# Kernel optimization log

Hardware: AMD Instinct MI355X
Metric: run time of the kernel (lower is better)

The kernel has to match this reference:

```python
import jax, jax.numpy as jnp
import numpy as np

B, T, S, H = 4, 256, 1024, 256


def setup_inputs() -> dict:
    key = jax.random.key(0)
    k1, k2, k3, k4, k5, k6 = jax.random.split(key, 6)
    query = jax.random.normal(k1, (B, T, H), dtype=jnp.float32)
    encoder_outputs = jax.random.normal(k2, (B, S, H), dtype=jnp.float32)
    src_lengths = jax.random.randint(k3, (B,), 1, S + 1).astype(jnp.int64)
    scale = 1.0 / np.sqrt(H)
    W_h = jax.random.normal(k4, (H, H), dtype=jnp.float32) * scale
    W_s = jax.random.normal(k5, (H, H), dtype=jnp.float32) * scale
    v = jax.random.normal(k6, (H,), dtype=jnp.float32) * scale
    return {
        "query": query,
        "encoder_outputs": encoder_outputs,
        "src_lengths": src_lengths,
        "W_h": W_h,
        "W_s": W_s,
        "v": v,
    }


def reference(query, encoder_outputs, src_lengths, W_h, W_s, v):
    # score(h_i, s_j) = v^T tanh(W_h h_i + W_s s_j)
    # project once per sequence, then broadcast-add over (tgt, src)
    q_proj = jnp.einsum("bth,hk->btk", query, W_h)            # (B, T, H)
    e_proj = jnp.einsum("bsh,hk->bsk", encoder_outputs, W_s)  # (B, S, H)
    # (B, T, S, H) additive intermediate -> reduce with v
    feats = jnp.tanh(q_proj[:, :, None, :] + e_proj[:, None, :, :])
    scores = jnp.einsum("btsh,h->bts", feats, v)              # (B, T, S)
    # mask padding positions (src positions >= src_lengths[b])
    valid = jnp.arange(scores.shape[-1])[None, :] < src_lengths[:, None]  # (B, S)
    scores = jnp.where(valid[:, None, :], scores, jnp.finfo(scores.dtype).min)
    attn = jax.nn.softmax(scores, axis=-1)                    # (B, T, S)
    attn_out = jnp.einsum("bts,bsh->bth", attn, encoder_outputs)  # (B, T, H)
    return attn_out
```

## Files before the change

### kernel.cpp

```cpp
#include <hip/hip_runtime.h>
#include <math.h>

#define NB 4
#define NT 256
#define NS 1024
#define NH 256
#define TT 2
#define SBK 128
#define NSQ (NS / SBK)
#define BS (NB * NS)

static constexpr float CTWO   = 2.8853900817779268f;
static constexpr float LOG2E  = 1.4426950408889634f;
static constexpr float ACLAMP = 62.0f;

__global__ __launch_bounds__(256) void proj_kernel(const float* __restrict__ Q,
                                                   const float* __restrict__ E,
                                                   const float* __restrict__ W_h,
                                                   const float* __restrict__ W_s,
                                                   float* __restrict__ tq,
                                                   float* __restrict__ te4) {
  __shared__ float As[32][68];
  __shared__ float Bs[32][68];
  const int tid = threadIdx.x;
  int r0 = blockIdx.x * 64;
  const int n0 = blockIdx.y * 64;
  const bool is_q = (r0 < NB * NT);
  const float* A;
  const float* W;
  if (is_q) { A = Q; W = W_h; }
  else      { A = E; W = W_s; r0 -= NB * NT; }
  const int tx = tid & 15;
  const int ty = tid >> 4;
  float acc[4][4] = {};
  for (int k0 = 0; k0 < NH; k0 += 32) {
    {
      const int r = tid >> 2;
      const int kq = (tid & 3) * 8;
      const float* src = A + (size_t)(r0 + r) * NH + k0 + kq;
      float4 v0 = *(const float4*)(src);
      float4 v1 = *(const float4*)(src + 4);
      As[kq + 0][r] = v0.x; As[kq + 1][r] = v0.y; As[kq + 2][r] = v0.z; As[kq + 3][r] = v0.w;
      As[kq + 4][r] = v1.x; As[kq + 5][r] = v1.y; As[kq + 6][r] = v1.z; As[kq + 7][r] = v1.w;
    }
    {
      const int k = tid >> 3;
      const int nq = (tid & 7) * 8;
      const float* src = W + (size_t)(k0 + k) * NH + n0 + nq;
      *(float4*)&Bs[k][nq]     = *(const float4*)(src);
      *(float4*)&Bs[k][nq + 4] = *(const float4*)(src + 4);
    }
    __syncthreads();
    #pragma unroll
    for (int k = 0; k < 32; ++k) {
      float4 a = *(const float4*)&As[k][ty * 4];
      float4 b = *(const float4*)&Bs[k][tx * 4];
      const float av[4] = {a.x, a.y, a.z, a.w};
      const float bv[4] = {b.x, b.y, b.z, b.w};
      #pragma unroll
      for (int i = 0; i < 4; ++i)
        #pragma unroll
        for (int j = 0; j < 4; ++j)
          acc[i][j] = fmaf(av[i], bv[j], acc[i][j]);
    }
    __syncthreads();
  }
  #pragma unroll
  for (int i = 0; i < 4; ++i) {
    float vals[4];
    #pragma unroll
    for (int j = 0; j < 4; ++j) {
      float x = acc[i][j] * CTWO;
      x = fminf(fmaxf(x, -ACLAMP), ACLAMP);
      vals[j] = __builtin_amdgcn_exp2f(x);
    }
    const int r = r0 + ty * 4 + i;
    if (is_q) {
      #pragma unroll
      for (int j = 0; j < 4; ++j)
        tq[(size_t)r * NH + n0 + tx * 4 + j] = vals[j];
    } else {
      const int h4 = (n0 >> 2) + tx;
      float4 w = {vals[0], vals[1], vals[2], vals[3]};
      *(float4*)&te4[((size_t)h4 * BS + r) * 4] = w;
    }
  }
}

#define PAIR(qa, ea, va, qb, eb, vb, ACC)                                  \
  {                                                                        \
    float ta = fmaf((qa), (ea), 1.0f);                                     \
    float tb = fmaf((qb), (eb), 1.0f);                                     \
    float num = fmaf((va), tb, (vb) * ta);                                 \
    float den = ta * tb;                                                   \
    ACC = fmaf(num, __builtin_amdgcn_rcpf(den), ACC);                      \
  }

__global__ __launch_bounds__(256) void attn_main_kernel(
    const float4* __restrict__ tqq,
    const float4* __restrict__ te4q,
    const float4* __restrict__ enc4,
    const int* __restrict__ src_len,
    const float4* __restrict__ vq,
    float4* __restrict__ po4, float* __restrict__ mbuf, float* __restrict__ lbuf) {
  __shared__ float p_lds[4][TT][SBK];
  const int tid = threadIdx.x;
  const int wid = tid >> 6;
  const int lane = tid & 63;
  const int bx = blockIdx.x;
  const int sq = wid * 2 + (bx & 1);
  const int b  = (bx >> 1) & 3;
  const int tt = bx >> 3;
  const int btbase = b * NT + tt * TT;
  const int s0 = sq * SBK;
  const int len = src_len[b];

  if (s0 >= len) {
    if (lane < TT) {
      mbuf[(size_t)(btbase + lane) * NSQ + sq] = -INFINITY;
      lbuf[(size_t)(btbase + lane) * NSQ + sq] = 0.f;
    }
    return;
  }

  float sumv;
  {
    float4 v4 = vq[lane];
    float sv = (v4.x + v4.y) + (v4.z + v4.w);
    #pragma unroll
    for (int o = 32; o > 0; o >>= 1) sv += __shfl_xor(sv, o, 64);
    sumv = sv;
  }

  const int gs0 = b * NS + s0;
  const int sa = s0 + lane;
  const int sb = s0 + 64 + lane;
  const bool va_ok = sa < len;
  const bool vb_ok = sb < len;

  float accA0[TT], accA1[TT], accB0[TT], accB1[TT];
  #pragma unroll
  for (int t = 0; t < TT; ++t) { accA0[t] = accA1[t] = accB0[t] = accB1[t] = 0.f; }

  #pragma unroll 4
  for (int h4 = 0; h4 < NH / 4; ++h4) {
    const float4 ea = te4q[(size_t)h4 * BS + gs0 + lane];
    const float4 eb = te4q[(size_t)h4 * BS + gs0 + 64 + lane];
    const float4 vv = vq[h4];
    #pragma unroll
    for (int t = 0; t < TT; ++t) {
      const float4 q = tqq[(size_t)(btbase + t) * (NH / 4) + h4];
      PAIR(q.x, ea.x, vv.x, q.y, ea.y, vv.y, accA0[t]);
      PAIR(q.z, ea.z, vv.z, q.w, ea.w, vv.w, accA1[t]);
      PAIR(q.x, eb.x, vv.x, q.y, eb.y, vv.y, accB0[t]);
      PAIR(q.z, eb.z, vv.z, q.w, eb.w, vv.w, accB1[t]);
    }
  }

  #pragma unroll
  for (int t = 0; t < TT; ++t) {
    float xa = va_ok ? fmaf(-2.f, accA0[t] + accA1[t], sumv) : -INFINITY;
    float xb = vb_ok ? fmaf(-2.f, accB0[t] + accB1[t], sumv) : -INFINITY;
    float m = fmaxf(xa, xb);
    #pragma unroll
    for (int o = 32; o > 0; o >>= 1) m = fmaxf(m, __shfl_xor(m, o, 64));
    float pa = __builtin_amdgcn_exp2f((xa - m) * LOG2E);
    float pb = __builtin_amdgcn_exp2f((xb - m) * LOG2E);
    float l = pa + pb;
    #pragma unroll
    for (int o = 32; o > 0; o >>= 1) l += __shfl_xor(l, o, 64);
    p_lds[wid][t][lane] = pa;
    p_lds[wid][t][64 + lane] = pb;
    if (lane == 0) {
      mbuf[(size_t)(btbase + t) * NSQ + sq] = m;
      lbuf[(size_t)(btbase + t) * NSQ + sq] = l;
    }
  }

  float4 o[TT];
  #pragma unroll
  for (int t = 0; t < TT; ++t) o[t] = make_float4(0.f, 0.f, 0.f, 0.f);
  #pragma unroll 2
  for (int s = 0; s < SBK; s += 4) {
    float4 e0 = enc4[(size_t)(gs0 + s + 0) * (NH / 4) + lane];
    float4 e1 = enc4[(size_t)(gs0 + s + 1) * (NH / 4) + lane];
    float4 e2 = enc4[(size_t)(gs0 + s + 2) * (NH / 4) + lane];
    float4 e3 = enc4[(size_t)(gs0 + s + 3) * (NH / 4) + lane];
    #pragma unroll
    for (int t = 0; t < TT; ++t) {
      float4 p = *(const float4*)&p_lds[wid][t][s];
      o[t].x = fmaf(p.x, e0.x, o[t].x); o[t].y = fmaf(p.x, e0.y, o[t].y);
      o[t].z = fmaf(p.x, e0.z, o[t].z); o[t].w = fmaf(p.x, e0.w, o[t].w);
      o[t].x = fmaf(p.y, e1.x, o[t].x); o[t].y = fmaf(p.y, e1.y, o[t].y);
      o[t].z = fmaf(p.y, e1.z, o[t].z); o[t].w = fmaf(p.y, e1.w, o[t].w);
      o[t].x = fmaf(p.z, e2.x, o[t].x); o[t].y = fmaf(p.z, e2.y, o[t].y);
      o[t].z = fmaf(p.z, e2.z, o[t].z); o[t].w = fmaf(p.z, e2.w, o[t].w);
      o[t].x = fmaf(p.w, e3.x, o[t].x); o[t].y = fmaf(p.w, e3.y, o[t].y);
      o[t].z = fmaf(p.w, e3.z, o[t].z); o[t].w = fmaf(p.w, e3.w, o[t].w);
    }
  }
  #pragma unroll
  for (int t = 0; t < TT; ++t)
    po4[((size_t)(btbase + t) * NSQ + sq) * (NH / 4) + lane] = o[t];
}

__global__ __launch_bounds__(256) void combine_kernel(const float* __restrict__ po,
                                                      const float* __restrict__ mbuf,
                                                      const float* __restrict__ lbuf,
                                                      float* __restrict__ out) {
  const int bt = blockIdx.x;
  const int h = threadIdx.x;
  float m[NSQ], l[NSQ];
  float M = -INFINITY;
  #pragma unroll
  for (int i = 0; i < NSQ; ++i) {
    m[i] = mbuf[(size_t)bt * NSQ + i];
    l[i] = lbuf[(size_t)bt * NSQ + i];
    M = fmaxf(M, m[i]);
  }
  float L = 0.f, o = 0.f;
  #pragma unroll
  for (int i = 0; i < NSQ; ++i) {
    if (m[i] > -INFINITY) {
      float w = __builtin_amdgcn_exp2f((m[i] - M) * LOG2E);
      L = fmaf(w, l[i], L);
      o = fmaf(w, po[((size_t)bt * NSQ + i) * NH + h], o);
    }
  }
  out[(size_t)bt * NH + h] = o / L;
}

extern "C" void kernel_launch(void* const* d_in, const int* in_sizes, int n_in,
                              void* d_out, int out_size, void* d_ws, size_t ws_size,
                              hipStream_t stream) {
  const float* query = (const float*)d_in[0];
  const float* enc   = (const float*)d_in[1];
  const int*   slen  = (const int*)d_in[2];
  const float* W_h   = (const float*)d_in[3];
  const float* W_s   = (const float*)d_in[4];
  const float* v     = (const float*)d_in[5];
  float* out = (float*)d_out;

  float* ws = (float*)d_ws;
  float* tq  = ws;
  float* te4 = tq + (size_t)NB * NT * NH;
  float* po  = te4 + (size_t)NB * NS * NH;
  float* mb  = po + (size_t)NB * NT * NSQ * NH;
  float* lb  = mb + (size_t)NB * NT * NSQ;

  hipLaunchKernelGGL(proj_kernel, dim3((NB * (NT + NS)) / 64, NH / 64), dim3(256), 0, stream,
                     query, enc, W_h, W_s, tq, te4);
  hipLaunchKernelGGL(attn_main_kernel, dim3(NB * (NT / TT) * NSQ / 4), dim3(256), 0, stream,
                     (const float4*)tq, (const float4*)te4, (const float4*)enc, slen,
                     (const float4*)v, (float4*)po, mb, lb);
  hipLaunchKernelGGL(combine_kernel, dim3(NB * NT), dim3(256), 0, stream, po, mb, lb, out);
}
```

Baseline: 73.88 us.

## Share encoder tiles across waves via LDS with direct global-to-LDS loads

Each block now covers 8 target rows and one source chunk, with its four waves sharing the same encoder projection and encoder tiles. Those tiles are staged in a 32 KB LDS buffer through global_load_lds, so each one is fetched once per block rather than once per wave. Block indexing is remapped so batches and source chunks interleave across the grid, and launch bounds now request 4 blocks per CU. The cost is extra barriers, higher LDS use that can lower occupancy, and a single buffer with no overlap between loads and compute.

Result: slower. 209.7 us (+183.9%).

```diff
diff --git a/kernel.cpp b/kernel.cpp
--- a/kernel.cpp
+++ b/kernel.cpp
@@ -5,6 +5,7 @@
 #define NT 256
 #define NS 1024
 #define NH 256
+#define BT 8
 #define TT 2
 #define SBK 128
 #define NSQ (NS / SBK)
@@ -13,6 +14,9 @@
 static constexpr float CTWO   = 2.8853900817779268f;
 static constexpr float LOG2E  = 1.4426950408889634f;
 static constexpr float ACLAMP = 62.0f;
+
+typedef __attribute__((address_space(1))) const void GAS;
+typedef __attribute__((address_space(3))) void LAS;
 
 __global__ __launch_bounds__(256) void proj_kernel(const float* __restrict__ Q,
                                                    const float* __restrict__ E,
@@ -96,29 +100,34 @@
     ACC = fmaf(num, __builtin_amdgcn_rcpf(den), ACC);                      \
   }
 
-__global__ __launch_bounds__(256) void attn_main_kernel(
+__global__ __launch_bounds__(256, 4) void attn_main_kernel(
     const float4* __restrict__ tqq,
     const float4* __restrict__ te4q,
     const float4* __restrict__ enc4,
     const int* __restrict__ src_len,
     const float4* __restrict__ vq,
     float4* __restrict__ po4, float* __restrict__ mbuf, float* __restrict__ lbuf) {
+  __shared__ float4 buf[2048];
   __shared__ float p_lds[4][TT][SBK];
   const int tid = threadIdx.x;
   const int wid = tid >> 6;
   const int lane = tid & 63;
   const int bx = blockIdx.x;
-  const int sq = wid * 2 + (bx & 1);
-  const int b  = (bx >> 1) & 3;
-  const int tt = bx >> 3;
-  const int btbase = b * NT + tt * TT;
+  const int x  = bx & 7;
+  const int j  = bx >> 3;
+  const int k  = j & 3;
+  const int tt8 = j >> 2;
+  const int b  = (x + k) & 3;
+  const int sq = (x >> 2) + 2 * k;
   const int s0 = sq * SBK;
   const int len = src_len[b];
+  const int btbase = b * NT + tt8 * BT;
+  const int wrow = btbase + wid * TT;
 
   if (s0 >= len) {
-    if (lane < TT) {
-      mbuf[(size_t)(btbase + lane) * NSQ + sq] = -INFINITY;
-      lbuf[(size_t)(btbase + lane) * NSQ + sq] = 0.f;
+    if (tid < BT) {
+      mbuf[(size_t)(btbase + tid) * NSQ + sq] = -INFINITY;
+      lbuf[(size_t)(btbase + tid) * NSQ + sq] = 0.f;
     }
     return;
   }
@@ -133,28 +142,37 @@
   }
 
   const int gs0 = b * NS + s0;
-  const int sa = s0 + lane;
-  const int sb = s0 + 64 + lane;
-  const bool va_ok = sa < len;
-  const bool vb_ok = sb < len;
+  const bool va_ok = (s0 + lane) < len;
+  const bool vb_ok = (s0 + 64 + lane) < len;
 
   float accA0[TT], accA1[TT], accB0[TT], accB1[TT];
   #pragma unroll
   for (int t = 0; t < TT; ++t) { accA0[t] = accA1[t] = accB0[t] = accB1[t] = 0.f; }
 
-  #pragma unroll 4
-  for (int h4 = 0; h4 < NH / 4; ++h4) {
-    const float4 ea = te4q[(size_t)h4 * BS + gs0 + lane];
-    const float4 eb = te4q[(size_t)h4 * BS + gs0 + 64 + lane];
-    const float4 vv = vq[h4];
-    #pragma unroll
-    for (int t = 0; t < TT; ++t) {
-      const float4 q = tqq[(size_t)(btbase + t) * (NH / 4) + h4];
-      PAIR(q.x, ea.x, vv.x, q.y, ea.y, vv.y, accA0[t]);
-      PAIR(q.z, ea.z, vv.z, q.w, ea.w, vv.w, accA1[t]);
-      PAIR(q.x, eb.x, vv.x, q.y, eb.y, vv.y, accB0[t]);
-      PAIR(q.z, eb.z, vv.z, q.w, eb.w, vv.w, accB1[t]);
-    }
+  for (int c = 0; c < 4; ++c) {
+    #pragma unroll
+    for (int i = 0; i < 8; ++i) {
+      const int f = tid + 256 * i;
+      const float4* src = &te4q[(size_t)(c * 16 + (f >> 7)) * BS + gs0 + (f & 127)];
+      __builtin_amdgcn_global_load_lds((GAS*)src, (LAS*)&buf[f], 16, 0, 0);
+    }
+    __syncthreads();
+    #pragma unroll
+    for (int h4c = 0; h4c < 16; ++h4c) {
+      const int h4 = c * 16 + h4c;
+      const float4 ea = buf[h4c * 128 + lane];
+      const float4 eb = buf[h4c * 128 + 64 + lane];
+      const float4 vv = vq[h4];
+      #pragma unroll
+      for (int t = 0; t < TT; ++t) {
+        const float4 q = tqq[(size_t)(wrow + t) * 64 + h4];
+        PAIR(q.x, ea.x, vv.x, q.y, ea.y, vv.y, accA0[t]);
+        PAIR(q.z, ea.z, vv.z, q.w, ea.w, vv.w, accA1[t]);
+        PAIR(q.x, eb.x, vv.x, q.y, eb.y, vv.y, accB0[t]);
+        PAIR(q.z, eb.z, vv.z, q.w, eb.w, vv.w, accB1[t]);
+      }
+    }
+    __syncthreads();
   }
 
   #pragma unroll
@@ -172,36 +190,39 @@
     p_lds[wid][t][lane] = pa;
     p_lds[wid][t][64 + lane] = pb;
     if (lane == 0) {
-      mbuf[(size_t)(btbase + t) * NSQ + sq] = m;
-      lbuf[(size_t)(btbase + t) * NSQ + sq] = l;
+      mbuf[(size_t)(wrow + t) * NSQ + sq] = m;
+      lbuf[(size_t)(wrow + t) * NSQ + sq] = l;
     }
   }
 
   float4 o[TT];
   #pragma unroll
   for (int t = 0; t < TT; ++t) o[t] = make_float4(0.f, 0.f, 0.f, 0.f);
-  #pragma unroll 2
-  for (int s = 0; s < SBK; s += 4) {
-    float4 e0 = enc4[(size_t)(gs0 + s + 0) * (NH / 4) + lane];
-    float4 e1 = enc4[(size_t)(gs0 + s + 1) * (NH / 4) + lane];
-    float4 e2 = enc4[(size_t)(gs0 + s + 2) * (NH / 4) + lane];
-    float4 e3 = enc4[(size_t)(gs0 + s + 3) * (NH / 4) + lane];
-    #pragma unroll
-    for (int t = 0; t < TT; ++t) {
-      float4 p = *(const float4*)&p_lds[wid][t][s];
-      o[t].x = fmaf(p.x, e0.x, o[t].x); o[t].y = fmaf(p.x, e0.y, o[t].y);
-      o[t].z = fmaf(p.x, e0.z, o[t].z); o[t].w = fmaf(p.x, e0.w, o[t].w);
-      o[t].x = fmaf(p.y, e1.x, o[t].x); o[t].y = fmaf(p.y, e1.y, o[t].y);
-      o[t].z = fmaf(p.y, e1.z, o[t].z); o[t].w = fmaf(p.y, e1.w, o[t].w);
-      o[t].x = fmaf(p.z, e2.x, o[t].x); o[t].y = fmaf(p.z, e2.y, o[t].y);
-      o[t].z = fmaf(p.z, e2.z, o[t].z); o[t].w = fmaf(p.z, e2.w, o[t].w);
-      o[t].x = fmaf(p.w, e3.x, o[t].x); o[t].y = fmaf(p.w, e3.y, o[t].y);
-      o[t].z = fmaf(p.w, e3.z, o[t].z); o[t].w = fmaf(p.w, e3.w, o[t].w);
-    }
+  for (int c = 0; c < 4; ++c) {
+    #pragma unroll
+    for (int i = 0; i < 8; ++i) {
+      const int f = tid + 256 * i;
+      const float4* src = &enc4[(size_t)(gs0 + c * 32 + (f >> 6)) * 64 + (f & 63)];
+      __builtin_amdgcn_global_load_lds((GAS*)src, (LAS*)&buf[f], 16, 0, 0);
+    }
+    __syncthreads();
+    #pragma unroll 8
+    for (int s = 0; s < 32; ++s) {
+      const float4 e = buf[s * 64 + lane];
+      #pragma unroll
+      for (int t = 0; t < TT; ++t) {
+        const float p = p_lds[wid][t][c * 32 + s];
+        o[t].x = fmaf(p, e.x, o[t].x);
+        o[t].y = fmaf(p, e.y, o[t].y);
+        o[t].z = fmaf(p, e.z, o[t].z);
+        o[t].w = fmaf(p, e.w, o[t].w);
+      }
+    }
+    __syncthreads();
   }
   #pragma unroll
   for (int t = 0; t < TT; ++t)
-    po4[((size_t)(btbase + t) * NSQ + sq) * (NH / 4) + lane] = o[t];
+    po4[((size_t)(wrow + t) * NSQ + sq) * (NH / 4) + lane] = o[t];
 }
 
 __global__ __launch_bounds__(256) void combine_kernel(const float* __restrict__ po,
@@ -250,7 +271,7 @@
 
   hipLaunchKernelGGL(proj_kernel, dim3((NB * (NT + NS)) / 64, NH / 64), dim3(256), 0, stream,
                      query, enc, W_h, W_s, tq, te4);
-  hipLaunchKernelGGL(attn_main_kernel, dim3(NB * (NT / TT) * NSQ / 4), dim3(256), 0, stream,
+  hipLaunchKernelGGL(attn_main_kernel, dim3(NB * (NT / BT) * NSQ), dim3(256), 0, stream,
                      (const float4*)tq, (const float4*)te4, (const float4*)enc, slen,
                      (const float4*)v, (float4*)po, mb, lb);
   hipLaunchKernelGGL(combine_kernel, dim3(NB * NT), dim3(256), 0, stream, po, mb, lb, out);
```

## Split hidden-dim reduction across waves and rebalance block-to-tile mapping

Applied to the files above, without the earlier changes.

Each block now handles one source chunk for four target rows. Its four waves split the hidden dimension in halves and combine partial scores through LDS with a barrier, where before each wave owned its own source chunk. Block indices are swizzled so the chunks past the source length (which exit early) are spread evenly across consecutive blocks. This creates more blocks with finer-grained work to improve load balance and occupancy, at the cost of extra LDS traffic, two __syncthreads, and a weighted-sum loop with less register reuse of the encoder rows.

Result: slower. 101.8 us (+37.8%).

```diff
diff --git a/kernel.cpp b/kernel.cpp
--- a/kernel.cpp
+++ b/kernel.cpp
@@ -5,7 +5,7 @@
 #define NT 256
 #define NS 1024
 #define NH 256
-#define TT 2
+#define BT 4
 #define SBK 128
 #define NSQ (NS / SBK)
 #define BS (NB * NS)
@@ -103,22 +103,24 @@
     const int* __restrict__ src_len,
     const float4* __restrict__ vq,
     float4* __restrict__ po4, float* __restrict__ mbuf, float* __restrict__ lbuf) {
-  __shared__ float p_lds[4][TT][SBK];
+  __shared__ float part[2][BT][SBK];
+  __shared__ float p_lds[BT][SBK];
   const int tid = threadIdx.x;
   const int wid = tid >> 6;
   const int lane = tid & 63;
   const int bx = blockIdx.x;
-  const int sq = wid * 2 + (bx & 1);
-  const int b  = (bx >> 1) & 3;
-  const int tt = bx >> 3;
-  const int btbase = b * NT + tt * TT;
+  const int low5 = bx & 31;
+  const int b  = low5 & 3;
+  const int sq = ((low5 >> 2) + 2 * b) & 7;
+  const int tg = bx >> 5;
+  const int btbase = b * NT + tg * BT;
   const int s0 = sq * SBK;
   const int len = src_len[b];
 
   if (s0 >= len) {
-    if (lane < TT) {
-      mbuf[(size_t)(btbase + lane) * NSQ + sq] = -INFINITY;
-      lbuf[(size_t)(btbase + lane) * NSQ + sq] = 0.f;
+    if (tid < BT) {
+      mbuf[(size_t)(btbase + tid) * NSQ + sq] = -INFINITY;
+      lbuf[(size_t)(btbase + tid) * NSQ + sq] = 0.f;
     }
     return;
   }
@@ -133,34 +135,44 @@
   }
 
   const int gs0 = b * NS + s0;
-  const int sa = s0 + lane;
-  const int sb = s0 + 64 + lane;
-  const bool va_ok = sa < len;
-  const bool vb_ok = sb < len;
-
-  float accA0[TT], accA1[TT], accB0[TT], accB1[TT];
-  #pragma unroll
-  for (int t = 0; t < TT; ++t) { accA0[t] = accA1[t] = accB0[t] = accB1[t] = 0.f; }
-
-  #pragma unroll 4
-  for (int h4 = 0; h4 < NH / 4; ++h4) {
-    const float4 ea = te4q[(size_t)h4 * BS + gs0 + lane];
-    const float4 eb = te4q[(size_t)h4 * BS + gs0 + 64 + lane];
-    const float4 vv = vq[h4];
-    #pragma unroll
-    for (int t = 0; t < TT; ++t) {
-      const float4 q = tqq[(size_t)(btbase + t) * (NH / 4) + h4];
-      PAIR(q.x, ea.x, vv.x, q.y, ea.y, vv.y, accA0[t]);
-      PAIR(q.z, ea.z, vv.z, q.w, ea.w, vv.w, accA1[t]);
-      PAIR(q.x, eb.x, vv.x, q.y, eb.y, vv.y, accB0[t]);
-      PAIR(q.z, eb.z, vv.z, q.w, eb.w, vv.w, accB1[t]);
-    }
-  }
-
-  #pragma unroll
-  for (int t = 0; t < TT; ++t) {
-    float xa = va_ok ? fmaf(-2.f, accA0[t] + accA1[t], sumv) : -INFINITY;
-    float xb = vb_ok ? fmaf(-2.f, accB0[t] + accB1[t], sumv) : -INFINITY;
+
+  {
+    const int tp = wid >> 1;
+    const int hh = wid & 1;
+    float accA[2] = {0.f, 0.f};
+    float accB[2] = {0.f, 0.f};
+    const int h4base = hh * 32;
+    #pragma unroll 8
+    for (int i = 0; i < 32; ++i) {
+      const int h4 = h4base + i;
+      const float4 ea = te4q[(size_t)h4 * BS + gs0 + lane];
+      const float4 eb = te4q[(size_t)h4 * BS + gs0 + 64 + lane];
+      const float4 vv = vq[h4];
+      #pragma unroll
+      for (int t = 0; t < 2; ++t) {
+        const float4 q = tqq[(size_t)(btbase + tp * 2 + t) * 64 + h4];
+        PAIR(q.x, ea.x, vv.x, q.y, ea.y, vv.y, accA[t]);
+        PAIR(q.z, ea.z, vv.z, q.w, ea.w, vv.w, accA[t]);
+        PAIR(q.x, eb.x, vv.x, q.y, eb.y, vv.y, accB[t]);
+        PAIR(q.z, eb.z, vv.z, q.w, eb.w, vv.w, accB[t]);
+      }
+    }
+    #pragma unroll
+    for (int t = 0; t < 2; ++t) {
+      part[hh][tp * 2 + t][lane]      = accA[t];
+      part[hh][tp * 2 + t][64 + lane] = accB[t];
+    }
+  }
+  __syncthreads();
+
+  const int r = wid;
+  {
+    const bool va_ok = (s0 + lane) < len;
+    const bool vb_ok = (s0 + 64 + lane) < len;
+    float sa = part[0][r][lane]      + part[1][r][lane];
+    float sb = part[0][r][64 + lane] + part[1][r][64 + lane];
+    float xa = va_ok ? fmaf(-2.f, sa, sumv) : -INFINITY;
+    float xb = vb_ok ? fmaf(-2.f, sb, sumv) : -INFINITY;
     float m = fmaxf(xa, xb);
     #pragma unroll
     for (int o = 32; o > 0; o >>= 1) m = fmaxf(m, __shfl_xor(m, o, 64));
@@ -169,39 +181,28 @@
     float l = pa + pb;
     #pragma unroll
     for (int o = 32; o > 0; o >>= 1) l += __shfl_xor(l, o, 64);
-    p_lds[wid][t][lane] = pa;
-    p_lds[wid][t][64 + lane] = pb;
+    p_lds[r][lane] = pa;
+    p_lds[r][64 + lane] = pb;
     if (lane == 0) {
-      mbuf[(size_t)(btbase + t) * NSQ + sq] = m;
-      lbuf[(size_t)(btbase + t) * NSQ + sq] = l;
-    }
-  }
-
-  float4 o[TT];
-  #pragma unroll
-  for (int t = 0; t < TT; ++t) o[t] = make_float4(0.f, 0.f, 0.f, 0.f);
-  #pragma unroll 2
-  for (int s = 0; s < SBK; s += 4) {
-    float4 e0 = enc4[(size_t)(gs0 + s + 0) * (NH / 4) + lane];
-    float4 e1 = enc4[(size_t)(gs0 + s + 1) * (NH / 4) + lane];
-    float4 e2 = enc4[(size_t)(gs0 + s + 2) * (NH / 4) + lane];
-    float4 e3 = enc4[(size_t)(gs0 + s + 3) * (NH / 4) + lane];
-    #pragma unroll
-    for (int t = 0; t < TT; ++t) {
-      float4 p = *(const float4*)&p_lds[wid][t][s];
-      o[t].x = fmaf(p.x, e0.x, o[t].x); o[t].y = fmaf(p.x, e0.y, o[t].y);
-      o[t].z = fmaf(p.x, e0.z, o[t].z); o[t].w = fmaf(p.x, e0.w, o[t].w);
-      o[t].x = fmaf(p.y, e1.x, o[t].x); o[t].y = fmaf(p.y, e1.y, o[t].y);
-      o[t].z = fmaf(p.y, e1.z, o[t].z); o[t].w = fmaf(p.y, e1.w, o[t].w);
-      o[t].x = fmaf(p.z, e2.x, o[t].x); o[t].y = fmaf(p.z, e2.y, o[t].y);
-      o[t].z = fmaf(p.z, e2.z, o[t].z); o[t].w = fmaf(p.z, e2.w, o[t].w);
-      o[t].x = fmaf(p.w, e3.x, o[t].x); o[t].y = fmaf(p.w, e3.y, o[t].y);
-      o[t].z = fmaf(p.w, e3.z, o[t].z); o[t].w = fmaf(p.w, e3.w, o[t].w);
-    }
-  }
-  #pragma unroll
-  for (int t = 0; t < TT; ++t)
-    po4[((size_t)(btbase + t) * NSQ + sq) * (NH / 4) + lane] = o[t];
+      mbuf[(size_t)(btbase + r) * NSQ + sq] = m;
+      lbuf[(size_t)(btbase + r) * NSQ + sq] = l;
+    }
+  }
+  __syncthreads();
+
+  {
+    float4 o = make_float4(0.f, 0.f, 0.f, 0.f);
+    #pragma unroll 8
+    for (int s = 0; s < SBK; ++s) {
+      const float4 e = enc4[(size_t)(gs0 + s) * 64 + lane];
+      const float pp = p_lds[r][s];
+      o.x = fmaf(pp, e.x, o.x);
+      o.y = fmaf(pp, e.y, o.y);
+      o.z = fmaf(pp, e.z, o.z);
+      o.w = fmaf(pp, e.w, o.w);
+    }
+    po4[((size_t)(btbase + r) * NSQ + sq) * (NH / 4) + lane] = o;
+  }
 }
 
 __global__ __launch_bounds__(256) void combine_kernel(const float* __restrict__ po,
@@ -250,7 +251,7 @@
 
   hipLaunchKernelGGL(proj_kernel, dim3((NB * (NT + NS)) / 64, NH / 64), dim3(256), 0, stream,
                      query, enc, W_h, W_s, tq, te4);
-  hipLaunchKernelGGL(attn_main_kernel, dim3(NB * (NT / TT) * NSQ / 4), dim3(256), 0, stream,
+  hipLaunchKernelGGL(attn_main_kernel, dim3(NB * NSQ * (NT / BT)), dim3(256), 0, stream,
                      (const float4*)tq, (const float4*)te4, (const float4*)enc, slen,
                      (const float4*)v, (float4*)po, mb, lb);
   hipLaunchKernelGGL(combine_kernel, dim3(NB * NT), dim3(256), 0, stream, po, mb, lb, out);
```
